# Optimization experiments

Measured on AMD Instinct MI355X. Metric: run time of the kernel, lower is better.

## Reference

```python
import jax, jax.numpy as jnp
import numpy as np

K = 3        # dcn filter size
STRIDE = 2
PAD = 1
NEG_SLOPE = 0.1


def conv2d(x, w, stride, pad):
    return jax.lax.conv_general_dilated(
        x, w, (stride, stride), [(pad, pad), (pad, pad)],
        dimension_numbers=('NCHW', 'OIHW', 'NCHW'))


def setup_inputs() -> dict:
    key = jax.random.key(0)
    ks = jax.random.split(key, 6)
    N, H, W = 8, 256, 256
    return {
        'input_tensor': jax.random.normal(ks[0], (N, 3, H, W), jnp.float32),
        'conv1_w': jax.random.normal(ks[1], (8, 3, 1, 1), jnp.float32) * 0.3,
        'conv1_b': jax.random.normal(ks[2], (8,), jnp.float32) * 0.1,
        'offset_w': jax.random.normal(ks[3], (3 * K * K, 8, K, K), jnp.float32) * 0.05,
        'offset_b': jax.random.normal(ks[4], (3 * K * K,), jnp.float32) * 0.05,
        'dcn_w': jax.random.normal(ks[5], (512, 8, K, K), jnp.float32) * 0.1,
    }


def _dcnv2(x, offset_w, offset_b, dcn_w):
    # Modulated deformable conv v2 (bias_attr=False).
    N, C, H, W = x.shape
    K2 = K * K
    om = conv2d(x, offset_w, STRIDE, PAD) + offset_b[None, :, None, None]  # [N,3K2,Ho,Wo]
    offset = om[:, :2 * K2]
    mask = jax.nn.sigmoid(om[:, 2 * K2:])                                  # [N,K2,Ho,Wo]
    Ho, Wo = mask.shape[2], mask.shape[3]
    off = offset.reshape(N, K2, 2, Ho, Wo)  # (dy, dx) per kernel point
    dy, dx = off[:, :, 0], off[:, :, 1]
    ky, kx = jnp.meshgrid(jnp.arange(K), jnp.arange(K), indexing='ij')
    base_y = (jnp.arange(Ho) * STRIDE - PAD).astype(x.dtype)
    base_x = (jnp.arange(Wo) * STRIDE - PAD).astype(x.dtype)
    # Fractional sampling positions in input coordinates: [N,K2,Ho,Wo]
    py = base_y[None, None, :, None] + ky.reshape(-1)[None, :, None, None] + dy
    px = base_x[None, None, None, :] + kx.reshape(-1)[None, :, None, None] + dx
    # Bilinear sampling with zero padding outside the image.
    y0 = jnp.floor(py)
    x0 = jnp.floor(px)
    n_idx = jnp.arange(N)[:, None, None, None]
    cols = jnp.zeros((N, K2, Ho, Wo, C), x.dtype)
    for oy in (0.0, 1.0):
        for ox in (0.0, 1.0):
            yy = y0 + oy
            xx = x0 + ox
            w = (1.0 - jnp.abs(py - yy)) * (1.0 - jnp.abs(px - xx))
            valid = (yy >= 0) & (yy < H) & (xx >= 0) & (xx < W)
            iy = jnp.clip(yy, 0, H - 1).astype(jnp.int32)
            ix = jnp.clip(xx, 0, W - 1).astype(jnp.int32)
            # x[n_idx, :, iy, ix] -> [N,K2,Ho,Wo,C]
            cols = cols + jnp.where(valid, w, 0.0)[..., None] * x[n_idx, :, iy, ix]
    cols = cols * mask[..., None]  # modulation
    out_c = dcn_w.shape[0]
    return jnp.einsum('nkhwc,ock->nohw', cols, dcn_w.reshape(out_c, C, K2))


def reference(input_tensor, conv1_w, conv1_b, offset_w, offset_b, dcn_w):
    y = conv2d(input_tensor, conv1_w, 1, 0) + conv1_b[None, :, None, None]
    y = jnp.where(y >= 0, y, NEG_SLOPE * y)  # LeakyReLU(0.1)
    return _dcnv2(y, offset_w, offset_b, dcn_w)
```

## Files before the change

kernel.cpp:

```cpp
#include <hip/hip_runtime.h>
#include <math.h>

#define NB   8
#define HH   256
#define WW   256
#define CY   8
#define HO   128
#define WO   128
#define OCN  512
#define K2   9
#define KJ   72
#define KP   104

typedef short bf16x8 __attribute__((ext_vector_type(8)));
typedef float f32x4  __attribute__((ext_vector_type(4)));

static __device__ inline unsigned short f2bf(float f) {
    union { float f; unsigned u; } v; v.f = f;
    unsigned r = (v.u + 0x7FFFu + ((v.u >> 16) & 1u)) >> 16;
    return (unsigned short)r;
}

__global__ __launch_bounds__(256) void k_conv1(const float* __restrict__ x,
                                               const float* __restrict__ w,
                                               const float* __restrict__ b,
                                               float* __restrict__ y) {
    int idx = blockIdx.x * 256 + threadIdx.x;
    int n = idx >> 16, hw = idx & 65535;
    const float* xp = x + (size_t)n * 3 * 65536 + hw;
    float x0 = xp[0], x1 = xp[65536], x2 = xp[131072];
    float o[8];
#pragma unroll
    for (int oc = 0; oc < 8; ++oc) {
        float v = fmaf(w[oc*3+0], x0, fmaf(w[oc*3+1], x1, fmaf(w[oc*3+2], x2, b[oc])));
        o[oc] = v >= 0.f ? v : 0.1f * v;
    }
    float* yp = y + (size_t)idx * 8;
    *(float4*)(yp + 0) = make_float4(o[0], o[1], o[2], o[3]);
    *(float4*)(yp + 4) = make_float4(o[4], o[5], o[6], o[7]);
}

__global__ __launch_bounds__(256) void k_wpad(const float* __restrict__ wd,
                                              unsigned short* __restrict__ wdb) {
    int i = blockIdx.x * 256 + threadIdx.x;
    int row = i / KP;
    int k = i - row * KP;
    float v = (k < KJ) ? wd[row * KJ + k] : 0.f;
    wdb[i] = f2bf(v);
}

__global__ __launch_bounds__(256) void k_offset_sample(const float* __restrict__ y,
                                                       const float* __restrict__ ow,
                                                       const float* __restrict__ ob,
                                                       unsigned short* __restrict__ cols) {
    __shared__ __align__(16) unsigned short stage[256 * KP];

    int t = threadIdx.x;
    int idx = blockIdx.x * 256 + t;
    int n = idx >> 14, hw = idx & 16383;
    int ho = hw >> 7, wo = hw & 127;
    const float* yn = y + (size_t)n * (HH * WW * CY);

    float acc[27];
#pragma unroll
    for (int oc = 0; oc < 27; ++oc) acc[oc] = ob[oc];

#pragma unroll 1
    for (int pos = 0; pos < 9; ++pos) {
        int kh = pos / 3, kw = pos - kh * 3;
        int hi = 2 * ho - 1 + kh, wi = 2 * wo - 1 + kw;
        float4 a  = make_float4(0.f, 0.f, 0.f, 0.f);
        float4 c4 = make_float4(0.f, 0.f, 0.f, 0.f);
        if ((unsigned)hi < 256u && (unsigned)wi < 256u) {
            const float* yp = yn + ((size_t)hi * 256 + wi) * 8;
            a  = *(const float4*)(yp + 0);
            c4 = *(const float4*)(yp + 4);
        }
        const float* wp = ow + pos;
#pragma unroll
        for (int oc = 0; oc < 27; ++oc) {
            float s = fmaf(wp[oc*72 + 0*9], a.x,
                      fmaf(wp[oc*72 + 1*9], a.y,
                      fmaf(wp[oc*72 + 2*9], a.z,
                      fmaf(wp[oc*72 + 3*9], a.w,
                      fmaf(wp[oc*72 + 4*9], c4.x,
                      fmaf(wp[oc*72 + 5*9], c4.y,
                      fmaf(wp[oc*72 + 6*9], c4.z,
                           wp[oc*72 + 7*9] * c4.w)))))));
            acc[oc] += s;
        }
    }

#pragma unroll
    for (int k = 0; k < 9; ++k) {
        float dy = acc[2 * k], dx = acc[2 * k + 1];
        float m  = 1.f / (1.f + expf(-acc[18 + k]));
        float py = (float)(2 * ho - 1 + (k / 3)) + dy;
        float px = (float)(2 * wo - 1 + (k % 3)) + dx;
        float y0f = floorf(py), x0f = floorf(px);
        float fy = py - y0f, fx = px - x0f;
        int y0 = (int)y0f, x0 = (int)x0f;
        float s0=0,s1=0,s2=0,s3=0,s4=0,s5=0,s6=0,s7=0;
#pragma unroll
        for (int oy = 0; oy < 2; ++oy) {
#pragma unroll
            for (int ox = 0; ox < 2; ++ox) {
                int yy = y0 + oy, xx = x0 + ox;
                float wgt = (oy ? fy : 1.f - fy) * (ox ? fx : 1.f - fx);
                if ((unsigned)yy < 256u && (unsigned)xx < 256u) {
                    const float* yp = yn + ((size_t)yy * 256 + xx) * 8;
                    float4 a  = *(const float4*)(yp + 0);
                    float4 c4 = *(const float4*)(yp + 4);
                    s0 = fmaf(wgt, a.x,  s0); s1 = fmaf(wgt, a.y,  s1);
                    s2 = fmaf(wgt, a.z,  s2); s3 = fmaf(wgt, a.w,  s3);
                    s4 = fmaf(wgt, c4.x, s4); s5 = fmaf(wgt, c4.y, s5);
                    s6 = fmaf(wgt, c4.z, s6); s7 = fmaf(wgt, c4.w, s7);
                }
            }
        }
        unsigned short* sp = stage + t * KP + k;
        sp[0*9] = f2bf(m*s0); sp[1*9] = f2bf(m*s1); sp[2*9] = f2bf(m*s2); sp[3*9] = f2bf(m*s3);
        sp[4*9] = f2bf(m*s4); sp[5*9] = f2bf(m*s5); sp[6*9] = f2bf(m*s6); sp[7*9] = f2bf(m*s7);
    }
    {
        uint4 z; z.x = z.y = z.z = z.w = 0u;
        uint4* zp = (uint4*)((unsigned char*)stage + (size_t)t * 2 * KP + 144);
        zp[0] = z; zp[1] = z; zp[2] = z; zp[3] = z;
    }
    __syncthreads();
    const uint4* sL = (const uint4*)stage;
    uint4* gD = (uint4*)(cols + (size_t)blockIdx.x * 256 * KP);
#pragma unroll
    for (int i = 0; i < 13; ++i) {
        int c = t + i * 256;
        gD[c] = sL[c];
    }
}

__global__ __launch_bounds__(256) void k_gemm_mfma(const unsigned short* __restrict__ colsb,
                                                   const unsigned short* __restrict__ wdb,
                                                   float* __restrict__ out) {
    __shared__ __align__(16) unsigned short cT[128 * KP];
    int t = threadIdx.x;
    int pixtile = blockIdx.x;
    int octile  = blockIdx.y;

    {
        const uint4* g4 = (const uint4*)(colsb + (size_t)pixtile * 128 * KP);
        uint4* l4 = (uint4*)cT;
#pragma unroll
        for (int i = 0; i < 7; ++i) {
            int c = t + i * 256;
            if (c < 1664) l4[c] = g4[c];
        }
    }

    int wave = t >> 6, lane = t & 63;
    int lr = lane & 15, lk = lane >> 4;
    int ocb = octile * 128 + wave * 32;

    bf16x8 aF[2][3];
#pragma unroll
    for (int m = 0; m < 2; ++m)
#pragma unroll
        for (int kk = 0; kk < 3; ++kk)
            aF[m][kk] = *(const bf16x8*)(wdb + (size_t)(ocb + m * 16 + lr) * KP + kk * 32 + lk * 8);

    __syncthreads();

    f32x4 acc[2][8];
#pragma unroll
    for (int m = 0; m < 2; ++m)
#pragma unroll
        for (int n = 0; n < 8; ++n) acc[m][n] = (f32x4){0.f, 0.f, 0.f, 0.f};

#pragma unroll
    for (int kk = 0; kk < 3; ++kk) {
        bf16x8 bF[8];
#pragma unroll
        for (int n = 0; n < 8; ++n)
            bF[n] = *(const bf16x8*)(cT + (n * 16 + lr) * KP + kk * 32 + lk * 8);
#pragma unroll
        for (int n = 0; n < 8; ++n)
#pragma unroll
            for (int m = 0; m < 2; ++m)
                acc[m][n] = __builtin_amdgcn_mfma_f32_16x16x32_bf16(aF[m][kk], bF[n], acc[m][n], 0, 0, 0);
    }

    int pix0 = pixtile * 128;
    int nimg = pix0 >> 14;
    int hwbase = pix0 & 16383;
#pragma unroll
    for (int m = 0; m < 2; ++m) {
        int oc = ocb + m * 16 + lk * 4;
#pragma unroll
        for (int n = 0; n < 8; ++n) {
            int hw = hwbase + n * 16 + lr;
            float* op = out + ((size_t)nimg * OCN + oc) * 16384 + hw;
            op[0]         = acc[m][n][0];
            op[16384]     = acc[m][n][1];
            op[2 * 16384] = acc[m][n][2];
            op[3 * 16384] = acc[m][n][3];
        }
    }
}

extern "C" void kernel_launch(void* const* d_in, const int* in_sizes, int n_in,
                              void* d_out, int out_size, void* d_ws, size_t ws_size,
                              hipStream_t stream) {
    const float* x   = (const float*)d_in[0];
    const float* c1w = (const float*)d_in[1];
    const float* c1b = (const float*)d_in[2];
    const float* ow  = (const float*)d_in[3];
    const float* ob  = (const float*)d_in[4];
    const float* dw  = (const float*)d_in[5];
    float* out = (float*)d_out;

    float* y = (float*)d_ws;
    unsigned short* colsb = (unsigned short*)((unsigned char*)d_ws + 16777216);
    unsigned short* wdb   = (unsigned short*)((unsigned char*)d_ws + 16777216 + 27262976);

    hipLaunchKernelGGL(k_conv1, dim3(2048), dim3(256), 0, stream, x, c1w, c1b, y);
    hipLaunchKernelGGL(k_wpad, dim3(208), dim3(256), 0, stream, dw, wdb);
    hipLaunchKernelGGL(k_offset_sample, dim3(512), dim3(256), 0, stream, y, ow, ob, colsb);
    hipLaunchKernelGGL(k_gemm_mfma, dim3(1024, 4), dim3(256), 0, stream, colsb, wdb, out);
}
```

Before: 335.3 us.

## Fuse offset/sampling stage into MFMA GEMM kernel, dropping cols buffer roundtrip

Merges the offset-conv plus bilinear sampling kernel with the bf16 MFMA GEMM. Each 512-thread block now builds a 128-pixel column tile in LDS and then computes all 512 output channels in two passes. This removes the global write and re-read of the cols buffer and one kernel launch. In exchange only 128 of 512 threads do the sampling phase, so the other waves sit idle there. Output stores are also made nontemporal.

```diff
diff --git a/kernel.cpp b/kernel.cpp
--- a/kernel.cpp
+++ b/kernel.cpp
@@ -49,158 +49,130 @@
     wdb[i] = f2bf(v);
 }
 
-__global__ __launch_bounds__(256) void k_offset_sample(const float* __restrict__ y,
-                                                       const float* __restrict__ ow,
-                                                       const float* __restrict__ ob,
-                                                       unsigned short* __restrict__ cols) {
-    __shared__ __align__(16) unsigned short stage[256 * KP];
+__global__ __launch_bounds__(512, 4) void k_fused(const float* __restrict__ y,
+                                                  const float* __restrict__ ow,
+                                                  const float* __restrict__ ob,
+                                                  const unsigned short* __restrict__ wdb,
+                                                  float* __restrict__ out) {
+    __shared__ __align__(16) unsigned short cT[128 * KP];
 
     int t = threadIdx.x;
-    int idx = blockIdx.x * 256 + t;
-    int n = idx >> 14, hw = idx & 16383;
-    int ho = hw >> 7, wo = hw & 127;
-    const float* yn = y + (size_t)n * (HH * WW * CY);
+    int pix0 = blockIdx.x * 128;
+    int nimg = pix0 >> 14;
+    int ho   = (pix0 & 16383) >> 7;
+    const float* yn = y + (size_t)nimg * (HH * WW * CY);
 
-    float acc[27];
+    if (t < 128) {
+        int wo = t;
+        float acc[27];
 #pragma unroll
-    for (int oc = 0; oc < 27; ++oc) acc[oc] = ob[oc];
+        for (int oc = 0; oc < 27; ++oc) acc[oc] = ob[oc];
 
 #pragma unroll 1
-    for (int pos = 0; pos < 9; ++pos) {
-        int kh = pos / 3, kw = pos - kh * 3;
-        int hi = 2 * ho - 1 + kh, wi = 2 * wo - 1 + kw;
-        float4 a  = make_float4(0.f, 0.f, 0.f, 0.f);
-        float4 c4 = make_float4(0.f, 0.f, 0.f, 0.f);
-        if ((unsigned)hi < 256u && (unsigned)wi < 256u) {
-            const float* yp = yn + ((size_t)hi * 256 + wi) * 8;
-            a  = *(const float4*)(yp + 0);
-            c4 = *(const float4*)(yp + 4);
+        for (int pos = 0; pos < 9; ++pos) {
+            int kh = pos / 3, kw = pos - kh * 3;
+            int hi = 2 * ho - 1 + kh, wi = 2 * wo - 1 + kw;
+            float4 a  = make_float4(0.f, 0.f, 0.f, 0.f);
+            float4 c4 = make_float4(0.f, 0.f, 0.f, 0.f);
+            if ((unsigned)hi < 256u && (unsigned)wi < 256u) {
+                const float* yp = yn + ((size_t)hi * 256 + wi) * 8;
+                a  = *(const float4*)(yp + 0);
+                c4 = *(const float4*)(yp + 4);
+            }
+            const float* wp = ow + pos;
+#pragma unroll
+            for (int oc = 0; oc < 27; ++oc) {
+                float s = fmaf(wp[oc*72 + 0*9], a.x,
+                          fmaf(wp[oc*72 + 1*9], a.y,
+                          fmaf(wp[oc*72 + 2*9], a.z,
+                          fmaf(wp[oc*72 + 3*9], a.w,
+                          fmaf(wp[oc*72 + 4*9], c4.x,
+                          fmaf(wp[oc*72 + 5*9], c4.y,
+                          fmaf(wp[oc*72 + 6*9], c4.z,
+                               wp[oc*72 + 7*9] * c4.w)))))));
+                acc[oc] += s;
+            }
         }
-        const float* wp = ow + pos;
+
 #pragma unroll
-        for (int oc = 0; oc < 27; ++oc) {
-            float s = fmaf(wp[oc*72 + 0*9], a.x,
-                      fmaf(wp[oc*72 + 1*9], a.y,
-                      fmaf(wp[oc*72 + 2*9], a.z,
-                      fmaf(wp[oc*72 + 3*9], a.w,
-                      fmaf(wp[oc*72 + 4*9], c4.x,
-                      fmaf(wp[oc*72 + 5*9], c4.y,
-                      fmaf(wp[oc*72 + 6*9], c4.z,
-                           wp[oc*72 + 7*9] * c4.w)))))));
-            acc[oc] += s;
+        for (int k = 0; k < 9; ++k) {
+            float dy = acc[2 * k], dx = acc[2 * k + 1];
+            float m  = 1.f / (1.f + expf(-acc[18 + k]));
+            float py = (float)(2 * ho - 1 + (k / 3)) + dy;
+            float px = (float)(2 * wo - 1 + (k % 3)) + dx;
+            float y0f = floorf(py), x0f = floorf(px);
+            float fy = py - y0f, fx = px - x0f;
+            int y0 = (int)y0f, x0 = (int)x0f;
+            float s0=0,s1=0,s2=0,s3=0,s4=0,s5=0,s6=0,s7=0;
+#pragma unroll
+            for (int oy = 0; oy < 2; ++oy) {
+#pragma unroll
+                for (int ox = 0; ox < 2; ++ox) {
+                    int yy = y0 + oy, xx = x0 + ox;
+                    float wgt = (oy ? fy : 1.f - fy) * (ox ? fx : 1.f - fx);
+                    if ((unsigned)yy < 256u && (unsigned)xx < 256u) {
+                        const float* yp = yn + ((size_t)yy * 256 + xx) * 8;
+                        float4 a  = *(const float4*)(yp + 0);
+                        float4 c4 = *(const float4*)(yp + 4);
+                        s0 = fmaf(wgt, a.x,  s0); s1 = fmaf(wgt, a.y,  s1);
+                        s2 = fmaf(wgt, a.z,  s2); s3 = fmaf(wgt, a.w,  s3);
+                        s4 = fmaf(wgt, c4.x, s4); s5 = fmaf(wgt, c4.y, s5);
+                        s6 = fmaf(wgt, c4.z, s6); s7 = fmaf(wgt, c4.w, s7);
+                    }
+                }
+            }
+            unsigned short* cp = cT + t * KP + k;
+            cp[0*9] = f2bf(m*s0); cp[1*9] = f2bf(m*s1); cp[2*9] = f2bf(m*s2); cp[3*9] = f2bf(m*s3);
+            cp[4*9] = f2bf(m*s4); cp[5*9] = f2bf(m*s5); cp[6*9] = f2bf(m*s6); cp[7*9] = f2bf(m*s7);
+        }
+        {
+            uint4 z; z.x = z.y = z.z = z.w = 0u;
+            uint4* zp = (uint4*)((unsigned char*)cT + (size_t)t * 2 * KP + 144);
+            zp[0] = z; zp[1] = z; zp[2] = z; zp[3] = z;
         }
     }
+    __syncthreads();
+
+    int wave = t >> 6, lane = t & 63, lr = lane & 15, lk = lane >> 4;
+    int hwbase = pix0 & 16383;
+#pragma unroll
+    for (int p = 0; p < 2; ++p) {
+        int ocb = p * 256 + wave * 32;
+        bf16x8 aF[2][3];
+#pragma unroll
+        for (int m = 0; m < 2; ++m)
+#pragma unroll
+            for (int kk = 0; kk < 3; ++kk)
+                aF[m][kk] = *(const bf16x8*)(wdb + (size_t)(ocb + m * 16 + lr) * KP + kk * 32 + lk * 8);
+
+        f32x4 acc2[2][8];
+#pragma unroll
+        for (int m = 0; m < 2; ++m)
+#pragma unroll
+            for (int n = 0; n < 8; ++n) acc2[m][n] = (f32x4){0.f, 0.f, 0.f, 0.f};
 
 #pragma unroll
-    for (int k = 0; k < 9; ++k) {
-        float dy = acc[2 * k], dx = acc[2 * k + 1];
-        float m  = 1.f / (1.f + expf(-acc[18 + k]));
-        float py = (float)(2 * ho - 1 + (k / 3)) + dy;
-        float px = (float)(2 * wo - 1 + (k % 3)) + dx;
-        float y0f = floorf(py), x0f = floorf(px);
-        float fy = py - y0f, fx = px - x0f;
-        int y0 = (int)y0f, x0 = (int)x0f;
-        float s0=0,s1=0,s2=0,s3=0,s4=0,s5=0,s6=0,s7=0;
+        for (int kk = 0; kk < 3; ++kk) {
 #pragma unroll
-        for (int oy = 0; oy < 2; ++oy) {
-#pragma unroll
-            for (int ox = 0; ox < 2; ++ox) {
-                int yy = y0 + oy, xx = x0 + ox;
-                float wgt = (oy ? fy : 1.f - fy) * (ox ? fx : 1.f - fx);
-                if ((unsigned)yy < 256u && (unsigned)xx < 256u) {
-                    const float* yp = yn + ((size_t)yy * 256 + xx) * 8;
-                    float4 a  = *(const float4*)(yp + 0);
-                    float4 c4 = *(const float4*)(yp + 4);
-                    s0 = fmaf(wgt, a.x,  s0); s1 = fmaf(wgt, a.y,  s1);
-                    s2 = fmaf(wgt, a.z,  s2); s3 = fmaf(wgt, a.w,  s3);
-                    s4 = fmaf(wgt, c4.x, s4); s5 = fmaf(wgt, c4.y, s5);
-                    s6 = fmaf(wgt, c4.z, s6); s7 = fmaf(wgt, c4.w, s7);
-                }
+            for (int n = 0; n < 8; ++n) {
+                bf16x8 bF = *(const bf16x8*)(cT + (n * 16 + lr) * KP + kk * 32 + lk * 8);
+                acc2[0][n] = __builtin_amdgcn_mfma_f32_16x16x32_bf16(aF[0][kk], bF, acc2[0][n], 0, 0, 0);
+                acc2[1][n] = __builtin_amdgcn_mfma_f32_16x16x32_bf16(aF[1][kk], bF, acc2[1][n], 0, 0, 0);
             }
         }
-        unsigned short* sp = stage + t * KP + k;
-        sp[0*9] = f2bf(m*s0); sp[1*9] = f2bf(m*s1); sp[2*9] = f2bf(m*s2); sp[3*9] = f2bf(m*s3);
-        sp[4*9] = f2bf(m*s4); sp[5*9] = f2bf(m*s5); sp[6*9] = f2bf(m*s6); sp[7*9] = f2bf(m*s7);
-    }
-    {
-        uint4 z; z.x = z.y = z.z = z.w = 0u;
-        uint4* zp = (uint4*)((unsigned char*)stage + (size_t)t * 2 * KP + 144);
-        zp[0] = z; zp[1] = z; zp[2] = z; zp[3] = z;
-    }
-    __syncthreads();
-    const uint4* sL = (const uint4*)stage;
-    uint4* gD = (uint4*)(cols + (size_t)blockIdx.x * 256 * KP);
-#pragma unroll
-    for (int i = 0; i < 13; ++i) {
-        int c = t + i * 256;
-        gD[c] = sL[c];
-    }
-}
-
-__global__ __launch_bounds__(256) void k_gemm_mfma(const unsigned short* __restrict__ colsb,
-                                                   const unsigned short* __restrict__ wdb,
-                                                   float* __restrict__ out) {
-    __shared__ __align__(16) unsigned short cT[128 * KP];
-    int t = threadIdx.x;
-    int pixtile = blockIdx.x;
-    int octile  = blockIdx.y;
-
-    {
-        const uint4* g4 = (const uint4*)(colsb + (size_t)pixtile * 128 * KP);
-        uint4* l4 = (uint4*)cT;
-#pragma unroll
-        for (int i = 0; i < 7; ++i) {
-            int c = t + i * 256;
-            if (c < 1664) l4[c] = g4[c];
-        }
-    }
-
-    int wave = t >> 6, lane = t & 63;
-    int lr = lane & 15, lk = lane >> 4;
-    int ocb = octile * 128 + wave * 32;
-
-    bf16x8 aF[2][3];
-#pragma unroll
-    for (int m = 0; m < 2; ++m)
-#pragma unroll
-        for (int kk = 0; kk < 3; ++kk)
-            aF[m][kk] = *(const bf16x8*)(wdb + (size_t)(ocb + m * 16 + lr) * KP + kk * 32 + lk * 8);
-
-    __syncthreads();
-
-    f32x4 acc[2][8];
-#pragma unroll
-    for (int m = 0; m < 2; ++m)
-#pragma unroll
-        for (int n = 0; n < 8; ++n) acc[m][n] = (f32x4){0.f, 0.f, 0.f, 0.f};
 
 #pragma unroll
-    for (int kk = 0; kk < 3; ++kk) {
-        bf16x8 bF[8];
+        for (int m = 0; m < 2; ++m) {
+            int oc = ocb + m * 16 + lk * 4;
 #pragma unroll
-        for (int n = 0; n < 8; ++n)
-            bF[n] = *(const bf16x8*)(cT + (n * 16 + lr) * KP + kk * 32 + lk * 8);
-#pragma unroll
-        for (int n = 0; n < 8; ++n)
-#pragma unroll
-            for (int m = 0; m < 2; ++m)
-                acc[m][n] = __builtin_amdgcn_mfma_f32_16x16x32_bf16(aF[m][kk], bF[n], acc[m][n], 0, 0, 0);
-    }
-
-    int pix0 = pixtile * 128;
-    int nimg = pix0 >> 14;
-    int hwbase = pix0 & 16383;
-#pragma unroll
-    for (int m = 0; m < 2; ++m) {
-        int oc = ocb + m * 16 + lk * 4;
-#pragma unroll
-        for (int n = 0; n < 8; ++n) {
-            int hw = hwbase + n * 16 + lr;
-            float* op = out + ((size_t)nimg * OCN + oc) * 16384 + hw;
-            op[0]         = acc[m][n][0];
-            op[16384]     = acc[m][n][1];
-            op[2 * 16384] = acc[m][n][2];
-            op[3 * 16384] = acc[m][n][3];
+            for (int n = 0; n < 8; ++n) {
+                int hw = hwbase + n * 16 + lr;
+                float* op = out + ((size_t)nimg * OCN + oc) * 16384 + hw;
+                __builtin_nontemporal_store(acc2[m][n][0], op);
+                __builtin_nontemporal_store(acc2[m][n][1], op + 16384);
+                __builtin_nontemporal_store(acc2[m][n][2], op + 2 * 16384);
+                __builtin_nontemporal_store(acc2[m][n][3], op + 3 * 16384);
+            }
         }
     }
 }
@@ -216,12 +188,10 @@
     const float* dw  = (const float*)d_in[5];
     float* out = (float*)d_out;
 
-    float* y = (float*)d_ws;
-    unsigned short* colsb = (unsigned short*)((unsigned char*)d_ws + 16777216);
-    unsigned short* wdb   = (unsigned short*)((unsigned char*)d_ws + 16777216 + 27262976);
+    float* yb = (float*)d_ws;
+    unsigned short* wdb = (unsigned short*)((unsigned char*)d_ws + 16777216);
 
-    hipLaunchKernelGGL(k_conv1, dim3(2048), dim3(256), 0, stream, x, c1w, c1b, y);
+    hipLaunchKernelGGL(k_conv1, dim3(2048), dim3(256), 0, stream, x, c1w, c1b, yb);
     hipLaunchKernelGGL(k_wpad, dim3(208), dim3(256), 0, stream, dw, wdb);
-    hipLaunchKernelGGL(k_offset_sample, dim3(512), dim3(256), 0, stream, y, ow, ob, colsb);
-    hipLaunchKernelGGL(k_gemm_mfma, dim3(1024, 4), dim3(256), 0, stream, colsb, wdb, out);
+    hipLaunchKernelGGL(k_fused, dim3(1024), dim3(512), 0, stream, yb, ow, ob, wdb, out);
 }
```

Measured after the change: 340.2 us. No clear change (+1.4%).
